# Kernel optimization log

Hardware: AMD Instinct MI355X
Metric: run time of the kernel (lower is better)

Reference implementation:

```python
import jax, jax.numpy as jnp
import numpy as np

N, D, H, B, HID, E = 4096, 64, 4, 4, 64, 32768
NEG_SLOPE = 0.2


def setup_inputs() -> dict:
    key = jax.random.key(0)
    ks = jax.random.split(key, 24)
    s = 0.05
    emb = jax.random.normal(ks[0], (N, D), jnp.float32)
    src = jax.random.randint(ks[1], (E,), 0, N)
    dst = jax.random.randint(ks[2], (E,), 0, N)
    bond = jax.random.randint(ks[3], (E,), 0, B)
    # append self-loops (bond type 0) so every softmax row has a finite entry
    loop = jnp.arange(N)
    src = jnp.concatenate([src, loop])
    dst = jnp.concatenate([dst, loop])
    bond = jnp.concatenate([bond, jnp.zeros((N,), bond.dtype)])
    return {
        'embeddings': emb,
        'Qw': jax.random.normal(ks[4], (D, D), jnp.float32) * s,
        'Qb': jnp.zeros((D,), jnp.float32),
        'Kw': jax.random.normal(ks[5], (D, D), jnp.float32) * s,
        'Kb': jnp.zeros((D,), jnp.float32),
        'Vw': jax.random.normal(ks[6], (D, D), jnp.float32) * s,
        'Vb': jnp.zeros((D,), jnp.float32),
        'W0': jax.random.normal(ks[7], (B, H, 2 * D, HID), jnp.float32) * s,
        'b0': jnp.zeros((B, H, HID), jnp.float32),
        'W1': jax.random.normal(ks[8], (B, H, HID, HID), jnp.float32) * s,
        'b1': jnp.zeros((B, H, HID), jnp.float32),
        'W2': jax.random.normal(ks[9], (B, H, HID), jnp.float32) * s,
        'b2': jnp.zeros((B, H), jnp.float32),
        'Pw': jax.random.normal(ks[10], (H * D, D), jnp.float32) * s,
        'Pb': jnp.zeros((D,), jnp.float32),
        'src': src,
        'dst': dst,
        'bond': bond,
    }


def reference(embeddings, Qw, Qb, Kw, Kb, Vw, Vb, W0, b0, W1, b1, W2, b2, Pw, Pb, src, dst, bond):
    n, d = embeddings.shape
    nb, nh = W0.shape[0], W0.shape[1]
    Q = embeddings @ Qw + Qb
    K = embeddings @ Kw + Kb
    V = embeddings @ Vw + Vb
    # symmetric scatter: scores for both (src->dst) and (dst->src)
    s_all = jnp.concatenate([src, dst])
    d_all = jnp.concatenate([dst, src])
    b_all = jnp.concatenate([bond, bond])
    x = jnp.concatenate([Q[s_all], K[d_all]], axis=-1)  # [2E', 2D]

    def mlp_scores(bt):
        h = jax.nn.relu(jnp.einsum('ef,hfk->ehk', x, W0[bt]) + b0[bt])
        h = jax.nn.relu(jnp.einsum('ehk,hkj->ehj', h, W1[bt]) + b1[bt])
        sc = jnp.einsum('ehk,hk->eh', h, W2[bt]) + b2[bt]
        return jax.nn.leaky_relu(sc, NEG_SLOPE)

    scores = jnp.zeros((x.shape[0], nh), x.dtype)
    for bt in range(nb):  # small fixed loop over bond types (grouped GEMMs)
        scores = jnp.where((b_all == bt)[:, None], mlp_scores(bt), scores)

    S = jnp.full((nh, n, n), -jnp.inf, embeddings.dtype)
    S = S.at[:, s_all, d_all].set(scores.T)  # [H, N, N]
    A = jax.nn.softmax(S, axis=-1)
    out = jnp.einsum('hij,jd->hid', A, V)  # [H, N, D]
    out = out.transpose(1, 0, 2).reshape(n, nh * d)
    return out @ Pw + Pb
```

## Files before the change

### kernel.cpp

```cpp
#include <hip/hip_runtime.h>
#include <hip/hip_bf16.h>
#include <math.h>

#define D 64
#define H 4
#define NB 4
#define TILE 64
#define PAD 128
#define NEG_SLOPE 0.2f

typedef __attribute__((ext_vector_type(8))) short short8;
typedef __attribute__((ext_vector_type(4))) float f32x4;

__device__ __forceinline__ unsigned short f2bf(float f) {
    union { float f; unsigned int u; } c; c.f = f;
    const unsigned int u = c.u;
    return (unsigned short)((u + 0x7fffu + ((u >> 16) & 1u)) >> 16);
}

__global__ __launch_bounds__(256) void prep_kernel(
    const float* __restrict__ emb,
    const float* __restrict__ Qw, const float* __restrict__ Qb,
    const float* __restrict__ Kw, const float* __restrict__ Kb,
    const float* __restrict__ Vw, const float* __restrict__ Vb,
    unsigned short* __restrict__ Qbf, unsigned short* __restrict__ Kbf,
    float* __restrict__ V,
    const float* __restrict__ W0, const float* __restrict__ W1,
    unsigned short* __restrict__ W0p, unsigned short* __restrict__ W1p,
    const int* __restrict__ bond, int Ep, int TE,
    int* __restrict__ rowFill, int* __restrict__ blockBondCnt, int nblk,
    int N, int nq8)
{
    __shared__ __align__(16) unsigned char pbuf[51200];
    const int tid = threadIdx.x;
    const int bid = blockIdx.x;
    if (bid < nq8) {
        float* wq = (float*)pbuf;
        float* wk = (float*)(pbuf + 16384);
        float* wv = (float*)(pbuf + 32768);
        float* et = (float*)(pbuf + 49152);
        const int base_n = bid * 8;
        if (tid < 8 && base_n + tid < N) rowFill[base_n + tid] = 0;
        {
            const float4* q4 = (const float4*)Qw;
            const float4* k4 = (const float4*)Kw;
            const float4* v4 = (const float4*)Vw;
            float4* wq4 = (float4*)wq;
            float4* wk4 = (float4*)wk;
            float4* wv4 = (float4*)wv;
            for (int i = tid; i < 1024; i += 256) {
                wq4[i] = q4[i];
                wk4[i] = k4[i];
                wv4[i] = v4[i];
            }
        }
        for (int i = tid; i < 512; i += 256) {
            const int n = base_n + (i >> 6);
            et[i] = (n < N) ? emb[n * D + (i & 63)] : 0.f;
        }
        __syncthreads();
        const int lane = tid & 63, wave = tid >> 6;
        const int d = lane;
#pragma unroll
        for (int r = 0; r < 2; ++r) {
            const int li = r * 4 + wave;
            const int n = base_n + li;
            if (n < N) {
                float aq = Qb[d], ak = Kb[d], av = Vb[d];
                const float* er = et + li * 64;
#pragma unroll 8
                for (int k = 0; k < D; ++k) {
                    const float x = er[k];
                    aq += x * wq[k * D + d];
                    ak += x * wk[k * D + d];
                    av += x * wv[k * D + d];
                }
                Qbf[n * D + d] = f2bf(aq);
                Kbf[n * D + d] = f2bf(ak);
                V[n * D + d] = av;
            }
        }
    } else if (bid < nq8 + 512) {
        const int idx = (bid - nq8) * 256 + tid;
        {
            const int j = idx & 7, ln = (idx >> 3) & 63, nt = (idx >> 9) & 3;
            const int ks = (idx >> 11) & 3, bh = idx >> 13;
            const int k = ks * 32 + ((ln >> 4) << 3) + j;
            const int nn = (nt << 4) + (ln & 15);
            W0p[idx] = f2bf(W0[((size_t)bh * 128 + k) * 64 + nn]);
        }
        if (idx < 65536) {
            const int j = idx & 7, ln = (idx >> 3) & 63, nt = (idx >> 9) & 3;
            const int ks = (idx >> 11) & 1, bh = idx >> 12;
            const int k = ks * 32 + ((ln >> 4) << 3) + j;
            const int nn = (nt << 4) + (ln & 15);
            W1p[idx] = f2bf(W1[((size_t)bh * 64 + k) * 64 + nn]);
        }
    } else {
        int* wcnt = (int*)pbuf;
        const int vb = bid - nq8 - 512;
        const int e = vb * 256 + tid;
        const int lane = tid & 63, wave = tid >> 6;
        int bt = -1;
        if (e < TE) bt = (e < Ep) ? bond[e] : bond[e - Ep];
#pragma unroll
        for (int t = 0; t < NB; ++t) {
            const unsigned long long m = __ballot(bt == t);
            if (lane == 0) wcnt[wave * NB + t] = (int)__popcll(m);
        }
        __syncthreads();
        if (tid < NB) {
            int s = 0;
#pragma unroll
            for (int w = 0; w < 4; ++w) s += wcnt[w * NB + tid];
            blockBondCnt[tid * nblk + vb] = s;
        }
    }
}

__global__ __launch_bounds__(256) void scatter_kernel(
    const int* __restrict__ src, const int* __restrict__ dst,
    const int* __restrict__ bond, int Ep, int TE, int nblk,
    const int* __restrict__ blockBondCnt, int* __restrict__ rowFill,
    int* __restrict__ edge_col, int* __restrict__ edge_eid,
    int* __restrict__ padPos, int* __restrict__ bond_edges, int* __restrict__ bondOff)
{
    __shared__ int chunkpre[256];
    __shared__ int base_lds[NB];
    __shared__ int wcnt[4][NB], wbase[4][NB];
    const int tid = threadIdx.x;
    const int vb = blockIdx.x;
    const int M = NB * nblk;
    const int c = (M + 255) >> 8;

    int s = 0;
    for (int i = 0; i < c; ++i) { const int idx = tid * c + i; if (idx < M) s += blockBondCnt[idx]; }
    chunkpre[tid] = s;
    __syncthreads();
    int val = s;
    for (int off = 1; off < 256; off <<= 1) {
        const int o = (tid >= off) ? chunkpre[tid - off] : 0;
        __syncthreads();
        val += o;
        chunkpre[tid] = val;
        __syncthreads();
    }
    int excl = val - s;
    for (int i = 0; i < c; ++i) {
        const int idx = tid * c + i;
        if (idx < M) {
            const int t = idx / nblk, r = idx - t * nblk;
            if (r == vb) base_lds[t] = excl;
            if (vb == 0 && r == 0) bondOff[t] = excl;
            excl += blockBondCnt[idx];
        }
    }
    if (vb == 0 && tid == 255) bondOff[NB] = chunkpre[255];
    __syncthreads();

    const int lane = tid & 63, wave = tid >> 6;
    const int e = vb * 256 + tid;
    const bool act = (e < TE);
    int sN = 0, dN = 0, bt = -1;
    if (act) {
        if (e < Ep) { sN = src[e]; dN = dst[e]; bt = bond[e]; }
        else        { sN = dst[e - Ep]; dN = src[e - Ep]; bt = bond[e - Ep]; }
        const int p = atomicAdd(&rowFill[sN], 1);
        if (p < PAD) {
            edge_col[sN * PAD + p] = dN;
            edge_eid[sN * PAD + p] = e;
            padPos[e] = sN * PAD + p;
        } else padPos[e] = -1;
    }
    int myrank = 0;
#pragma unroll
    for (int t = 0; t < NB; ++t) {
        const unsigned long long m = __ballot(bt == t);
        if (lane == 0) wcnt[wave][t] = (int)__popcll(m);
        if (bt == t) myrank = (int)__popcll(m & ((1ull << lane) - 1ull));
    }
    __syncthreads();
    if (tid < NB) {
        int sum = 0;
#pragma unroll
        for (int w = 0; w < 4; ++w) { wbase[w][tid] = sum; sum += wcnt[w][tid]; }
    }
    __syncthreads();
    if (act) bond_edges[base_lds[bt] + wbase[wave][bt] + myrank] = e;
}

__global__ __launch_bounds__(256) void mlp_kernel(
    const unsigned short* __restrict__ Qbf, const unsigned short* __restrict__ Kbf,
    const int* __restrict__ src, const int* __restrict__ dst, int Ep,
    const int* __restrict__ bondOff, const int* __restrict__ bond_edges,
    const int* __restrict__ padPos,
    const unsigned short* __restrict__ W0p, const unsigned short* __restrict__ W1p,
    const float* __restrict__ b0, const float* __restrict__ b1,
    const float* __restrict__ W2, const float* __restrict__ b2,
    float* __restrict__ S)
{
    const int bt = blockIdx.y;
    const int base = bondOff[bt];
    const int cnt  = bondOff[bt + 1] - base;
    const int t0 = blockIdx.x * TILE;
    if (t0 >= cnt) return;
    const int ne = min(TILE, cnt - t0);

    __shared__ __align__(16) unsigned char buf[32768];
    __shared__ int eids[TILE];

    const int tid = threadIdx.x;
    if (tid < TILE) eids[tid] = (tid < ne) ? bond_edges[base + t0 + tid] : 0;
    __syncthreads();

    for (int i = tid; i < 1024; i += 256) {
        const int el = i >> 4, u = i & 15;
        uint4 v = make_uint4(0, 0, 0, 0);
        if (el < ne) {
            const int e = eids[el];
            int s, d;
            if (e < Ep) { s = src[e]; d = dst[e]; }
            else        { s = dst[e - Ep]; d = src[e - Ep]; }
            v = (u < 8) ? ((const uint4*)(Qbf + s * 64))[u]
                        : ((const uint4*)(Kbf + d * 64))[u - 8];
        }
        const int b = (el << 8) + (u << 4);
        *(uint4*)(buf + (b ^ ((el & 7) << 4))) = v;
    }

    const int lane = tid & 63;
    const int h = tid >> 6;
    const int bh = bt * H + h;
    const int lg = lane >> 4;
    const int lr = lane & 15;

    const int e_w = ((lr >> 2) << 4) + (lg << 2) + (lr & 3);
    const int pp = (e_w < ne) ? padPos[eids[e_w]] : -1;
    __syncthreads();

    f32x4 acc[4][4];
    const float* bb0 = b0 + bh * 64;
#pragma unroll
    for (int nt = 0; nt < 4; ++nt) {
        const float bv = bb0[(nt << 4) + lr];
#pragma unroll
        for (int mt = 0; mt < 4; ++mt) acc[mt][nt] = (f32x4){bv, bv, bv, bv};
    }
    const short8* W0f = (const short8*)W0p + (size_t)bh * 1024;
#pragma unroll
    for (int ks = 0; ks < 4; ++ks) {
        short8 a[4];
        const int koff = (ks << 6) + (lg << 4);
#pragma unroll
        for (int mt = 0; mt < 4; ++mt) {
            const int row = (mt << 4) + lr;
            const int b = (row << 8) + koff;
            a[mt] = *(const short8*)(buf + (b ^ ((row & 7) << 4)));
        }
        short8 bfr[4];
#pragma unroll
        for (int nt = 0; nt < 4; ++nt) bfr[nt] = W0f[(((ks << 2) + nt) << 6) + lane];
#pragma unroll
        for (int mt = 0; mt < 4; ++mt)
#pragma unroll
            for (int nt = 0; nt < 4; ++nt)
                acc[mt][nt] = __builtin_amdgcn_mfma_f32_16x16x32_bf16(a[mt], bfr[nt], acc[mt][nt], 0, 0, 0);
    }
    __syncthreads();
    unsigned char* h0 = buf + h * 8192;
#pragma unroll
    for (int mt = 0; mt < 4; ++mt)
#pragma unroll
        for (int nt = 0; nt < 4; ++nt)
#pragma unroll
            for (int r = 0; r < 4; ++r) {
                const int row = (mt << 4) + (lg << 2) + r;
                const int col = (nt << 4) + lr;
                const int b = (row << 7) + (col << 1);
                *(unsigned short*)(h0 + (b ^ ((row & 7) << 4))) = f2bf(fmaxf(acc[mt][nt][r], 0.f));
            }

    f32x4 acc1[4][4];
    const float* bb1 = b1 + bh * 64;
#pragma unroll
    for (int nt = 0; nt < 4; ++nt) {
        const float bv = bb1[(nt << 4) + lr];
#pragma unroll
        for (int mt = 0; mt < 4; ++mt) acc1[mt][nt] = (f32x4){bv, bv, bv, bv};
    }
    const short8* W1f = (const short8*)W1p + (size_t)bh * 512;
#pragma unroll
    for (int ks = 0; ks < 2; ++ks) {
        short8 a[4];
        const int koff = (ks << 6) + (lg << 4);
#pragma unroll
        for (int mt = 0; mt < 4; ++mt) {
            const int row = (mt << 4) + lr;
            const int b = (row << 7) + koff;
            a[mt] = *(const short8*)(h0 + (b ^ ((row & 7) << 4)));
        }
        short8 bfr[4];
#pragma unroll
        for (int nt = 0; nt < 4; ++nt) bfr[nt] = W1f[(((ks << 2) + nt) << 6) + lane];
#pragma unroll
        for (int mt = 0; mt < 4; ++mt)
#pragma unroll
            for (int nt = 0; nt < 4; ++nt)
                acc1[mt][nt] = __builtin_amdgcn_mfma_f32_16x16x32_bf16(a[mt], bfr[nt], acc1[mt][nt], 0, 0, 0);
    }

    const float* w2 = W2 + bh * 64;
    float w2v[4];
#pragma unroll
    for (int nt = 0; nt < 4; ++nt) w2v[nt] = w2[(nt << 4) + lr];
    float p[4][4];
#pragma unroll
    for (int mt = 0; mt < 4; ++mt)
#pragma unroll
        for (int r = 0; r < 4; ++r) {
            float s = 0.f;
#pragma unroll
            for (int nt = 0; nt < 4; ++nt) s += fmaxf(acc1[mt][nt][r], 0.f) * w2v[nt];
            p[mt][r] = s;
        }
#pragma unroll
    for (int off = 1; off <= 8; off <<= 1)
#pragma unroll
        for (int mt = 0; mt < 4; ++mt)
#pragma unroll
            for (int r = 0; r < 4; ++r) p[mt][r] += __shfl_xor(p[mt][r], off, 64);
    float sc = p[lr >> 2][lr & 3] + b2[bh];
    sc = sc > 0.f ? sc : NEG_SLOPE * sc;
    if (e_w < ne && pp >= 0) S[(size_t)pp * H + h] = sc;
}

__global__ __launch_bounds__(256) void agg_kernel(
    const float* __restrict__ V, const float* __restrict__ S,
    const int* __restrict__ rowFill,
    const int* __restrict__ edge_col, const int* __restrict__ edge_eid,
    const float* __restrict__ Pw, const float* __restrict__ Pb, float* __restrict__ out)
{
    const int row = blockIdx.x;
    const int tid = threadIdx.x;
    const int lane = tid & 63;
    const int wv = tid >> 6;
    const int beg = row * PAD;
    int deg = rowFill[row];
    if (deg > PAD) deg = PAD;

    __shared__ int tcol[PAD], teid[PAD], scol[PAD], spos[PAD], win[PAD];
    __shared__ float wgt[4][PAD];
    __shared__ float sdn[4];
    __shared__ float partv[4][4][64];
    __shared__ float rr[256];
    __shared__ float part2[4][64];

    for (int a = tid; a < deg; a += 256) { tcol[a] = edge_col[beg + a]; teid[a] = edge_eid[beg + a]; }
    __syncthreads();
    for (int a = tid; a < deg; a += 256) {
        const int e = teid[a];
        int r = 0;
        for (int b = 0; b < deg; ++b) r += (teid[b] < e);
        scol[r] = tcol[a];
        spos[r] = a;
    }
    __syncthreads();
    for (int a = tid; a < deg; a += 256) {
        const int c = scol[a];
        int wn = 1;
        for (int b = a + 1; b < deg; ++b) if (scol[b] == c) { wn = 0; break; }
        win[a] = wn;
    }
    __syncthreads();

    float m = -1e30f;
    for (int a = lane; a < deg; a += 64)
        if (win[a]) m = fmaxf(m, S[(size_t)(beg + spos[a]) * H + wv]);
#pragma unroll
    for (int off = 32; off; off >>= 1) m = fmaxf(m, __shfl_xor(m, off, 64));

    float dn = 0.f;
    for (int a = lane; a < deg; a += 64) {
        const float wvv = win[a] ? __expf(S[(size_t)(beg + spos[a]) * H + wv] - m) : 0.f;
        wgt[wv][a] = wvv;
        dn += wvv;
    }
#pragma unroll
    for (int off = 32; off; off >>= 1) dn += __shfl_xor(dn, off, 64);
    if (lane == 0) sdn[wv] = dn;
    __syncthreads();

    float pv0 = 0.f, pv1 = 0.f, pv2 = 0.f, pv3 = 0.f;
    for (int a = wv; a < deg; a += 4) {
        const float vr = V[(size_t)scol[a] * D + lane];
        pv0 += wgt[0][a] * vr;
        pv1 += wgt[1][a] * vr;
        pv2 += wgt[2][a] * vr;
        pv3 += wgt[3][a] * vr;
    }
    partv[wv][0][lane] = pv0;
    partv[wv][1][lane] = pv1;
    partv[wv][2][lane] = pv2;
    partv[wv][3][lane] = pv3;
    __syncthreads();

    rr[wv * 64 + lane] = (partv[0][wv][lane] + partv[1][wv][lane]
                        + partv[2][wv][lane] + partv[3][wv][lane]) / sdn[wv];
    __syncthreads();

    {
        float sps = 0.f;
#pragma unroll 8
        for (int k = 0; k < 64; ++k) sps += rr[wv * 64 + k] * Pw[(wv * 64 + k) * D + lane];
        part2[wv][lane] = sps;
    }
    __syncthreads();
    if (tid < 64)
        out[(size_t)row * D + tid] = part2[0][tid] + part2[1][tid] + part2[2][tid] + part2[3][tid] + Pb[tid];
}

extern "C" void kernel_launch(void* const* d_in, const int* in_sizes, int n_in,
                              void* d_out, int out_size, void* d_ws, size_t ws_size,
                              hipStream_t stream)
{
    const float* emb = (const float*)d_in[0];
    const float* Qw  = (const float*)d_in[1];
    const float* Qb  = (const float*)d_in[2];
    const float* Kw  = (const float*)d_in[3];
    const float* Kb  = (const float*)d_in[4];
    const float* Vw  = (const float*)d_in[5];
    const float* Vb  = (const float*)d_in[6];
    const float* W0  = (const float*)d_in[7];
    const float* b0  = (const float*)d_in[8];
    const float* W1  = (const float*)d_in[9];
    const float* b1  = (const float*)d_in[10];
    const float* W2  = (const float*)d_in[11];
    const float* b2  = (const float*)d_in[12];
    const float* Pw  = (const float*)d_in[13];
    const float* Pb  = (const float*)d_in[14];
    const int* src   = (const int*)d_in[15];
    const int* dst   = (const int*)d_in[16];
    const int* bond  = (const int*)d_in[17];

    const int N  = in_sizes[0] / D;
    const int Ep = in_sizes[15];
    const int TE = 2 * Ep;
    const int nblk = (TE + 255) / 256;
    const int nq8 = (N + 7) / 8;

    char* w = (char*)d_ws;
    auto alloc = [&](size_t bytes) -> void* {
        void* p = (void*)w;
        w += ((bytes + 255) / 256) * 256;
        return p;
    };
    unsigned short* Qbf = (unsigned short*)alloc((size_t)N * D * 2);
    unsigned short* Kbf = (unsigned short*)alloc((size_t)N * D * 2);
    float* V        = (float*)alloc((size_t)N * D * 4);
    unsigned short* W0p = (unsigned short*)alloc((size_t)131072 * 2);
    unsigned short* W1p = (unsigned short*)alloc((size_t)65536 * 2);
    float* S        = (float*)alloc((size_t)N * PAD * H * 4);
    int* edge_col   = (int*)alloc((size_t)N * PAD * 4);
    int* edge_eid   = (int*)alloc((size_t)N * PAD * 4);
    int* bond_edges = (int*)alloc((size_t)TE * 4);
    int* padPos     = (int*)alloc((size_t)TE * 4);
    int* blockBondCnt = (int*)alloc((size_t)NB * nblk * 4);
    int* bondOff    = (int*)alloc((size_t)(NB + 1) * 4);
    int* rowFill    = (int*)alloc((size_t)N * 4);
    if ((size_t)(w - (char*)d_ws) > ws_size) return;

    prep_kernel<<<nq8 + 512 + nblk, 256, 0, stream>>>(
        emb, Qw, Qb, Kw, Kb, Vw, Vb, Qbf, Kbf, V, W0, W1, W0p, W1p,
        bond, Ep, TE, rowFill, blockBondCnt, nblk, N, nq8);
    scatter_kernel<<<nblk, 256, 0, stream>>>(
        src, dst, bond, Ep, TE, nblk, blockBondCnt, rowFill,
        edge_col, edge_eid, padPos, bond_edges, bondOff);
    dim3 mgrid((TE + TILE - 1) / TILE, NB);
    mlp_kernel<<<mgrid, 256, 0, stream>>>(
        Qbf, Kbf, src, dst, Ep, bondOff, bond_edges, padPos,
        W0p, W1p, b0, b1, W2, b2, S);
    agg_kernel<<<N, 256, 0, stream>>>(
        V, S, rowFill, edge_col, edge_eid, Pw, Pb, (float*)d_out);
}
```

Baseline: 76.44 us.

## Fuse bond bucketing and CSR scatter into MLP kernel, drop scatter kernel

Removes the global prefix-scan scatter kernel and the per-block bond counting. Each MLP block now compacts the edges of its own 256-edge chunk that match one bond type, using ballots in LDS. Extra blocks in the same launch fill the row adjacency lists. Scores are stored by edge id instead of padded position, so agg reads S[eid]. This saves one kernel launch and global passes, but a block may see under-full 64-row tiles since each chunk holds about 64 edges per bond, and reads of S in agg become scattered.

```diff
diff --git a/kernel.cpp b/kernel.cpp
--- a/kernel.cpp
+++ b/kernel.cpp
@@ -5,7 +5,6 @@
 #define D 64
 #define H 4
 #define NB 4
-#define TILE 64
 #define PAD 128
 #define NEG_SLOPE 0.2f
 
@@ -27,9 +26,7 @@
     float* __restrict__ V,
     const float* __restrict__ W0, const float* __restrict__ W1,
     unsigned short* __restrict__ W0p, unsigned short* __restrict__ W1p,
-    const int* __restrict__ bond, int Ep, int TE,
-    int* __restrict__ rowFill, int* __restrict__ blockBondCnt, int nblk,
-    int N, int nq8)
+    int* __restrict__ rowFill, int N, int nq8)
 {
     __shared__ __align__(16) unsigned char pbuf[51200];
     const int tid = threadIdx.x;
@@ -80,258 +77,208 @@
                 V[n * D + d] = av;
             }
         }
-    } else if (bid < nq8 + 512) {
-        const int idx = (bid - nq8) * 256 + tid;
-        {
+    } else {
+        const int base = (bid - nq8) * 1024;
+#pragma unroll
+        for (int kk = 0; kk < 4; ++kk) {
+            const int idx = base + kk * 256 + tid;
             const int j = idx & 7, ln = (idx >> 3) & 63, nt = (idx >> 9) & 3;
             const int ks = (idx >> 11) & 3, bh = idx >> 13;
             const int k = ks * 32 + ((ln >> 4) << 3) + j;
             const int nn = (nt << 4) + (ln & 15);
             W0p[idx] = f2bf(W0[((size_t)bh * 128 + k) * 64 + nn]);
         }
-        if (idx < 65536) {
+        const int base1 = (bid - nq8) * 512;
+#pragma unroll
+        for (int kk = 0; kk < 2; ++kk) {
+            const int idx = base1 + kk * 256 + tid;
             const int j = idx & 7, ln = (idx >> 3) & 63, nt = (idx >> 9) & 3;
             const int ks = (idx >> 11) & 1, bh = idx >> 12;
             const int k = ks * 32 + ((ln >> 4) << 3) + j;
             const int nn = (nt << 4) + (ln & 15);
             W1p[idx] = f2bf(W1[((size_t)bh * 64 + k) * 64 + nn]);
         }
-    } else {
-        int* wcnt = (int*)pbuf;
-        const int vb = bid - nq8 - 512;
-        const int e = vb * 256 + tid;
-        const int lane = tid & 63, wave = tid >> 6;
-        int bt = -1;
-        if (e < TE) bt = (e < Ep) ? bond[e] : bond[e - Ep];
-#pragma unroll
-        for (int t = 0; t < NB; ++t) {
-            const unsigned long long m = __ballot(bt == t);
-            if (lane == 0) wcnt[wave * NB + t] = (int)__popcll(m);
-        }
-        __syncthreads();
-        if (tid < NB) {
-            int s = 0;
-#pragma unroll
-            for (int w = 0; w < 4; ++w) s += wcnt[w * NB + tid];
-            blockBondCnt[tid * nblk + vb] = s;
-        }
     }
 }
 
-__global__ __launch_bounds__(256) void scatter_kernel(
+__global__ __launch_bounds__(256) void mlp_kernel(
+    const unsigned short* __restrict__ Qbf, const unsigned short* __restrict__ Kbf,
     const int* __restrict__ src, const int* __restrict__ dst,
     const int* __restrict__ bond, int Ep, int TE, int nblk,
-    const int* __restrict__ blockBondCnt, int* __restrict__ rowFill,
-    int* __restrict__ edge_col, int* __restrict__ edge_eid,
-    int* __restrict__ padPos, int* __restrict__ bond_edges, int* __restrict__ bondOff)
-{
-    __shared__ int chunkpre[256];
-    __shared__ int base_lds[NB];
-    __shared__ int wcnt[4][NB], wbase[4][NB];
-    const int tid = threadIdx.x;
-    const int vb = blockIdx.x;
-    const int M = NB * nblk;
-    const int c = (M + 255) >> 8;
-
-    int s = 0;
-    for (int i = 0; i < c; ++i) { const int idx = tid * c + i; if (idx < M) s += blockBondCnt[idx]; }
-    chunkpre[tid] = s;
-    __syncthreads();
-    int val = s;
-    for (int off = 1; off < 256; off <<= 1) {
-        const int o = (tid >= off) ? chunkpre[tid - off] : 0;
-        __syncthreads();
-        val += o;
-        chunkpre[tid] = val;
-        __syncthreads();
-    }
-    int excl = val - s;
-    for (int i = 0; i < c; ++i) {
-        const int idx = tid * c + i;
-        if (idx < M) {
-            const int t = idx / nblk, r = idx - t * nblk;
-            if (r == vb) base_lds[t] = excl;
-            if (vb == 0 && r == 0) bondOff[t] = excl;
-            excl += blockBondCnt[idx];
-        }
-    }
-    if (vb == 0 && tid == 255) bondOff[NB] = chunkpre[255];
-    __syncthreads();
-
-    const int lane = tid & 63, wave = tid >> 6;
-    const int e = vb * 256 + tid;
-    const bool act = (e < TE);
-    int sN = 0, dN = 0, bt = -1;
-    if (act) {
-        if (e < Ep) { sN = src[e]; dN = dst[e]; bt = bond[e]; }
-        else        { sN = dst[e - Ep]; dN = src[e - Ep]; bt = bond[e - Ep]; }
-        const int p = atomicAdd(&rowFill[sN], 1);
-        if (p < PAD) {
-            edge_col[sN * PAD + p] = dN;
-            edge_eid[sN * PAD + p] = e;
-            padPos[e] = sN * PAD + p;
-        } else padPos[e] = -1;
-    }
-    int myrank = 0;
-#pragma unroll
-    for (int t = 0; t < NB; ++t) {
-        const unsigned long long m = __ballot(bt == t);
-        if (lane == 0) wcnt[wave][t] = (int)__popcll(m);
-        if (bt == t) myrank = (int)__popcll(m & ((1ull << lane) - 1ull));
-    }
-    __syncthreads();
-    if (tid < NB) {
-        int sum = 0;
-#pragma unroll
-        for (int w = 0; w < 4; ++w) { wbase[w][tid] = sum; sum += wcnt[w][tid]; }
-    }
-    __syncthreads();
-    if (act) bond_edges[base_lds[bt] + wbase[wave][bt] + myrank] = e;
-}
-
-__global__ __launch_bounds__(256) void mlp_kernel(
-    const unsigned short* __restrict__ Qbf, const unsigned short* __restrict__ Kbf,
-    const int* __restrict__ src, const int* __restrict__ dst, int Ep,
-    const int* __restrict__ bondOff, const int* __restrict__ bond_edges,
-    const int* __restrict__ padPos,
+    int* __restrict__ rowFill, int* __restrict__ edge_col, int* __restrict__ edge_eid,
     const unsigned short* __restrict__ W0p, const unsigned short* __restrict__ W1p,
     const float* __restrict__ b0, const float* __restrict__ b1,
     const float* __restrict__ W2, const float* __restrict__ b2,
     float* __restrict__ S)
 {
-    const int bt = blockIdx.y;
-    const int base = bondOff[bt];
-    const int cnt  = bondOff[bt + 1] - base;
-    const int t0 = blockIdx.x * TILE;
-    if (t0 >= cnt) return;
-    const int ne = min(TILE, cnt - t0);
+    const int tid = threadIdx.x;
+    const int lane = tid & 63, wave = tid >> 6;
+
+    if (blockIdx.x >= nblk * NB) {
+        const int vb = blockIdx.x - nblk * NB;
+        const int e = vb * 256 + tid;
+        if (e < TE) {
+            int sN, dN;
+            if (e < Ep) { sN = src[e]; dN = dst[e]; }
+            else        { sN = dst[e - Ep]; dN = src[e - Ep]; }
+            const int p = atomicAdd(&rowFill[sN], 1);
+            if (p < PAD) {
+                edge_col[sN * PAD + p] = dN;
+                edge_eid[sN * PAD + p] = e;
+            }
+        }
+        return;
+    }
+
+    const int bt = blockIdx.x & (NB - 1);
+    const int vb = blockIdx.x >> 2;
 
     __shared__ __align__(16) unsigned char buf[32768];
-    __shared__ int eids[TILE];
-
-    const int tid = threadIdx.x;
-    if (tid < TILE) eids[tid] = (tid < ne) ? bond_edges[base + t0 + tid] : 0;
-    __syncthreads();
-
-    for (int i = tid; i < 1024; i += 256) {
-        const int el = i >> 4, u = i & 15;
-        uint4 v = make_uint4(0, 0, 0, 0);
-        if (el < ne) {
-            const int e = eids[el];
-            int s, d;
-            if (e < Ep) { s = src[e]; d = dst[e]; }
-            else        { s = dst[e - Ep]; d = src[e - Ep]; }
-            v = (u < 8) ? ((const uint4*)(Qbf + s * 64))[u]
-                        : ((const uint4*)(Kbf + d * 64))[u - 8];
-        }
-        const int b = (el << 8) + (u << 4);
-        *(uint4*)(buf + (b ^ ((el & 7) << 4))) = v;
-    }
-
-    const int lane = tid & 63;
-    const int h = tid >> 6;
+    __shared__ int glist[256];
+    __shared__ int wbase[5];
+
+    {
+        const int e = vb * 256 + tid;
+        int bmatch = 0;
+        if (e < TE) bmatch = ((e < Ep ? bond[e] : bond[e - Ep]) == bt) ? 1 : 0;
+        const unsigned long long m = __ballot(bmatch != 0);
+        const int rank = (int)__popcll(m & ((1ull << lane) - 1ull));
+        if (lane == 0) wbase[wave + 1] = (int)__popcll(m);
+        __syncthreads();
+        if (tid == 0) {
+            wbase[0] = 0;
+            for (int w_ = 1; w_ <= 4; ++w_) wbase[w_] += wbase[w_ - 1];
+        }
+        __syncthreads();
+        if (bmatch) glist[wbase[wave] + rank] = e;
+    }
+    __syncthreads();
+    const int ne_all = wbase[4];
+    if (ne_all == 0) return;
+
+    const int h = wave;
     const int bh = bt * H + h;
     const int lg = lane >> 4;
     const int lr = lane & 15;
-
     const int e_w = ((lr >> 2) << 4) + (lg << 2) + (lr & 3);
-    const int pp = (e_w < ne) ? padPos[eids[e_w]] : -1;
-    __syncthreads();
-
-    f32x4 acc[4][4];
+
+    const short8* W0f = (const short8*)W0p + (size_t)bh * 1024;
+    const short8* W1f = (const short8*)W1p + (size_t)bh * 512;
     const float* bb0 = b0 + bh * 64;
-#pragma unroll
-    for (int nt = 0; nt < 4; ++nt) {
-        const float bv = bb0[(nt << 4) + lr];
-#pragma unroll
-        for (int mt = 0; mt < 4; ++mt) acc[mt][nt] = (f32x4){bv, bv, bv, bv};
-    }
-    const short8* W0f = (const short8*)W0p + (size_t)bh * 1024;
-#pragma unroll
-    for (int ks = 0; ks < 4; ++ks) {
-        short8 a[4];
-        const int koff = (ks << 6) + (lg << 4);
-#pragma unroll
-        for (int mt = 0; mt < 4; ++mt) {
-            const int row = (mt << 4) + lr;
-            const int b = (row << 8) + koff;
-            a[mt] = *(const short8*)(buf + (b ^ ((row & 7) << 4)));
-        }
-        short8 bfr[4];
-#pragma unroll
-        for (int nt = 0; nt < 4; ++nt) bfr[nt] = W0f[(((ks << 2) + nt) << 6) + lane];
-#pragma unroll
-        for (int mt = 0; mt < 4; ++mt)
-#pragma unroll
-            for (int nt = 0; nt < 4; ++nt)
-                acc[mt][nt] = __builtin_amdgcn_mfma_f32_16x16x32_bf16(a[mt], bfr[nt], acc[mt][nt], 0, 0, 0);
-    }
-    __syncthreads();
-    unsigned char* h0 = buf + h * 8192;
-#pragma unroll
-    for (int mt = 0; mt < 4; ++mt)
-#pragma unroll
-        for (int nt = 0; nt < 4; ++nt)
-#pragma unroll
-            for (int r = 0; r < 4; ++r) {
-                const int row = (mt << 4) + (lg << 2) + r;
-                const int col = (nt << 4) + lr;
-                const int b = (row << 7) + (col << 1);
-                *(unsigned short*)(h0 + (b ^ ((row & 7) << 4))) = f2bf(fmaxf(acc[mt][nt][r], 0.f));
-            }
-
-    f32x4 acc1[4][4];
     const float* bb1 = b1 + bh * 64;
-#pragma unroll
-    for (int nt = 0; nt < 4; ++nt) {
-        const float bv = bb1[(nt << 4) + lr];
-#pragma unroll
-        for (int mt = 0; mt < 4; ++mt) acc1[mt][nt] = (f32x4){bv, bv, bv, bv};
-    }
-    const short8* W1f = (const short8*)W1p + (size_t)bh * 512;
-#pragma unroll
-    for (int ks = 0; ks < 2; ++ks) {
-        short8 a[4];
-        const int koff = (ks << 6) + (lg << 4);
-#pragma unroll
-        for (int mt = 0; mt < 4; ++mt) {
-            const int row = (mt << 4) + lr;
-            const int b = (row << 7) + koff;
-            a[mt] = *(const short8*)(h0 + (b ^ ((row & 7) << 4)));
-        }
-        short8 bfr[4];
-#pragma unroll
-        for (int nt = 0; nt < 4; ++nt) bfr[nt] = W1f[(((ks << 2) + nt) << 6) + lane];
-#pragma unroll
-        for (int mt = 0; mt < 4; ++mt)
-#pragma unroll
-            for (int nt = 0; nt < 4; ++nt)
-                acc1[mt][nt] = __builtin_amdgcn_mfma_f32_16x16x32_bf16(a[mt], bfr[nt], acc1[mt][nt], 0, 0, 0);
-    }
-
     const float* w2 = W2 + bh * 64;
     float w2v[4];
 #pragma unroll
     for (int nt = 0; nt < 4; ++nt) w2v[nt] = w2[(nt << 4) + lr];
-    float p[4][4];
-#pragma unroll
-    for (int mt = 0; mt < 4; ++mt)
-#pragma unroll
-        for (int r = 0; r < 4; ++r) {
-            float s = 0.f;
-#pragma unroll
-            for (int nt = 0; nt < 4; ++nt) s += fmaxf(acc1[mt][nt][r], 0.f) * w2v[nt];
-            p[mt][r] = s;
-        }
-#pragma unroll
-    for (int off = 1; off <= 8; off <<= 1)
+    const float b2v = b2[bh];
+
+    for (int st = 0; st * 64 < ne_all; ++st) {
+        const int ne = min(64, ne_all - st * 64);
+        __syncthreads();
+
+        for (int i = tid; i < 1024; i += 256) {
+            const int el = i >> 4, u = i & 15;
+            uint4 v = make_uint4(0, 0, 0, 0);
+            if (el < ne) {
+                const int e = glist[st * 64 + el];
+                int s, d;
+                if (e < Ep) { s = src[e]; d = dst[e]; }
+                else        { s = dst[e - Ep]; d = src[e - Ep]; }
+                v = (u < 8) ? ((const uint4*)(Qbf + s * 64))[u]
+                            : ((const uint4*)(Kbf + d * 64))[u - 8];
+            }
+            const int b = (el << 8) + (u << 4);
+            *(uint4*)(buf + (b ^ ((el & 7) << 4))) = v;
+        }
+        __syncthreads();
+
+        f32x4 acc[4][4];
+#pragma unroll
+        for (int nt = 0; nt < 4; ++nt) {
+            const float bv = bb0[(nt << 4) + lr];
+#pragma unroll
+            for (int mt = 0; mt < 4; ++mt) acc[mt][nt] = (f32x4){bv, bv, bv, bv};
+        }
+#pragma unroll
+        for (int ks = 0; ks < 4; ++ks) {
+            short8 a[4];
+            const int koff = (ks << 6) + (lg << 4);
+#pragma unroll
+            for (int mt = 0; mt < 4; ++mt) {
+                const int row = (mt << 4) + lr;
+                const int b = (row << 8) + koff;
+                a[mt] = *(const short8*)(buf + (b ^ ((row & 7) << 4)));
+            }
+            short8 bfr[4];
+#pragma unroll
+            for (int nt = 0; nt < 4; ++nt) bfr[nt] = W0f[(((ks << 2) + nt) << 6) + lane];
+#pragma unroll
+            for (int mt = 0; mt < 4; ++mt)
+#pragma unroll
+                for (int nt = 0; nt < 4; ++nt)
+                    acc[mt][nt] = __builtin_amdgcn_mfma_f32_16x16x32_bf16(a[mt], bfr[nt], acc[mt][nt], 0, 0, 0);
+        }
+        __syncthreads();
+        unsigned char* h0 = buf + h * 8192;
 #pragma unroll
         for (int mt = 0; mt < 4; ++mt)
 #pragma unroll
-            for (int r = 0; r < 4; ++r) p[mt][r] += __shfl_xor(p[mt][r], off, 64);
-    float sc = p[lr >> 2][lr & 3] + b2[bh];
-    sc = sc > 0.f ? sc : NEG_SLOPE * sc;
-    if (e_w < ne && pp >= 0) S[(size_t)pp * H + h] = sc;
+            for (int nt = 0; nt < 4; ++nt)
+#pragma unroll
+                for (int r = 0; r < 4; ++r) {
+                    const int row = (mt << 4) + (lg << 2) + r;
+                    const int col = (nt << 4) + lr;
+                    const int b = (row << 7) + (col << 1);
+                    *(unsigned short*)(h0 + (b ^ ((row & 7) << 4))) = f2bf(fmaxf(acc[mt][nt][r], 0.f));
+                }
+
+        f32x4 acc1[4][4];
+#pragma unroll
+        for (int nt = 0; nt < 4; ++nt) {
+            const float bv = bb1[(nt << 4) + lr];
+#pragma unroll
+            for (int mt = 0; mt < 4; ++mt) acc1[mt][nt] = (f32x4){bv, bv, bv, bv};
+        }
+#pragma unroll
+        for (int ks = 0; ks < 2; ++ks) {
+            short8 a[4];
+            const int koff = (ks << 6) + (lg << 4);
+#pragma unroll
+            for (int mt = 0; mt < 4; ++mt) {
+                const int row = (mt << 4) + lr;
+                const int b = (row << 7) + koff;
+                a[mt] = *(const short8*)(h0 + (b ^ ((row & 7) << 4)));
+            }
+            short8 bfr[4];
+#pragma unroll
+            for (int nt = 0; nt < 4; ++nt) bfr[nt] = W1f[(((ks << 2) + nt) << 6) + lane];
+#pragma unroll
+            for (int mt = 0; mt < 4; ++mt)
+#pragma unroll
+                for (int nt = 0; nt < 4; ++nt)
+                    acc1[mt][nt] = __builtin_amdgcn_mfma_f32_16x16x32_bf16(a[mt], bfr[nt], acc1[mt][nt], 0, 0, 0);
+        }
+
+        float p[4][4];
+#pragma unroll
+        for (int mt = 0; mt < 4; ++mt)
+#pragma unroll
+            for (int r = 0; r < 4; ++r) {
+                float s = 0.f;
+#pragma unroll
+                for (int nt = 0; nt < 4; ++nt) s += fmaxf(acc1[mt][nt][r], 0.f) * w2v[nt];
+                p[mt][r] = s;
+            }
+#pragma unroll
+        for (int off = 1; off <= 8; off <<= 1)
+#pragma unroll
+            for (int mt = 0; mt < 4; ++mt)
+#pragma unroll
+                for (int r = 0; r < 4; ++r) p[mt][r] += __shfl_xor(p[mt][r], off, 64);
+        float sc = p[lr >> 2][lr & 3] + b2v;
+        sc = sc > 0.f ? sc : NEG_SLOPE * sc;
+        if (e_w < ne) S[(size_t)glist[st * 64 + e_w] * H + h] = sc;
+    }
 }
 
 __global__ __launch_bounds__(256) void agg_kernel(
@@ -348,7 +295,7 @@
     int deg = rowFill[row];
     if (deg > PAD) deg = PAD;
 
-    __shared__ int tcol[PAD], teid[PAD], scol[PAD], spos[PAD], win[PAD];
+    __shared__ int tcol[PAD], teid[PAD], scol[PAD], seid[PAD], win[PAD];
     __shared__ float wgt[4][PAD];
     __shared__ float sdn[4];
     __shared__ float partv[4][4][64];
@@ -362,7 +309,7 @@
         int r = 0;
         for (int b = 0; b < deg; ++b) r += (teid[b] < e);
         scol[r] = tcol[a];
-        spos[r] = a;
+        seid[r] = e;
     }
     __syncthreads();
     for (int a = tid; a < deg; a += 256) {
@@ -375,13 +322,13 @@
 
     float m = -1e30f;
     for (int a = lane; a < deg; a += 64)
-        if (win[a]) m = fmaxf(m, S[(size_t)(beg + spos[a]) * H + wv]);
+        if (win[a]) m = fmaxf(m, S[(size_t)seid[a] * H + wv]);
 #pragma unroll
     for (int off = 32; off; off >>= 1) m = fmaxf(m, __shfl_xor(m, off, 64));
 
     float dn = 0.f;
     for (int a = lane; a < deg; a += 64) {
-        const float wvv = win[a] ? __expf(S[(size_t)(beg + spos[a]) * H + wv] - m) : 0.f;
+        const float wvv = win[a] ? __expf(S[(size_t)seid[a] * H + wv] - m) : 0.f;
         wgt[wv][a] = wvv;
         dn += wvv;
     }
@@ -459,25 +406,18 @@
     float* V        = (float*)alloc((size_t)N * D * 4);
     unsigned short* W0p = (unsigned short*)alloc((size_t)131072 * 2);
     unsigned short* W1p = (unsigned short*)alloc((size_t)65536 * 2);
-    float* S        = (float*)alloc((size_t)N * PAD * H * 4);
+    float* S        = (float*)alloc((size_t)TE * H * 4);
     int* edge_col   = (int*)alloc((size_t)N * PAD * 4);
     int* edge_eid   = (int*)alloc((size_t)N * PAD * 4);
-    int* bond_edges = (int*)alloc((size_t)TE * 4);
-    int* padPos     = (int*)alloc((size_t)TE * 4);
-    int* blockBondCnt = (int*)alloc((size_t)NB * nblk * 4);
-    int* bondOff    = (int*)alloc((size_t)(NB + 1) * 4);
     int* rowFill    = (int*)alloc((size_t)N * 4);
     if ((size_t)(w - (char*)d_ws) > ws_size) return;
 
-    prep_kernel<<<nq8 + 512 + nblk, 256, 0, stream>>>(
+    prep_kernel<<<nq8 + 128, 256, 0, stream>>>(
         emb, Qw, Qb, Kw, Kb, Vw, Vb, Qbf, Kbf, V, W0, W1, W0p, W1p,
-        bond, Ep, TE, rowFill, blockBondCnt, nblk, N, nq8);
-    scatter_kernel<<<nblk, 256, 0, stream>>>(
-        src, dst, bond, Ep, TE, nblk, blockBondCnt, rowFill,
-        edge_col, edge_eid, padPos, bond_edges, bondOff);
-    dim3 mgrid((TE + TILE - 1) / TILE, NB);
-    mlp_kernel<<<mgrid, 256, 0, stream>>>(
-        Qbf, Kbf, src, dst, Ep, bondOff, bond_edges, padPos,
+        rowFill, N, nq8);
+    mlp_kernel<<<nblk * NB + nblk, 256, 0, stream>>>(
+        Qbf, Kbf, src, dst, bond, Ep, TE, nblk,
+        rowFill, edge_col, edge_eid,
         W0p, W1p, b0, b1, W2, b2, S);
     agg_kernel<<<N, 256, 0, stream>>>(
         V, S, rowFill, edge_col, edge_eid, Pw, Pb, (float*)d_out);
```

Result: slower. 104.4 us (+36.6%).
